# Kernel optimization log

Measured on AMD Instinct MI355X. Metric: run time of the kernel, lower is better.

## Reference

```python
import jax, jax.numpy as jnp
import numpy as np

N_AXIS = 128      # n_x_axis == n_y_axis
N_TARGET = 8192


def setup_inputs() -> dict:
    key = jax.random.key(0)
    k1, k2 = jax.random.split(key, 2)
    # decoder output feature map: (4, n_y, n_x)
    feature_map = jax.random.normal(k1, (4, N_AXIS, N_AXIS), dtype=jnp.float32)
    # encoder grid: regular 2d grid in [-3, 3]^2, flattened (n_x*n_y, 2)
    ax = jnp.linspace(-3.0, 3.0, N_AXIS, dtype=jnp.float32)
    gx, gy = jnp.meshgrid(ax, ax, indexing='ij')
    grid = jnp.stack([gx, gy], axis=-1).reshape(N_AXIS * N_AXIS, 2)
    # target points in the same domain
    X_target = jax.random.uniform(k2, (N_TARGET, 2), dtype=jnp.float32,
                                  minval=-3.0, maxval=3.0)
    l_scale = jnp.float32(1.0)
    return {"feature_map": feature_map, "grid": grid,
            "X_target": X_target, "l_scale": l_scale}


def reference(feature_map, grid, X_target, l_scale):
    n_y, n_x = feature_map.shape[1], feature_map.shape[2]
    # Means_grid = FM[:2].permute(2,1,0).reshape(n_x*n_y, 2)
    means_grid = jnp.transpose(feature_map[:2], (2, 1, 0)).reshape(n_x * n_y, 2)
    # Sigmas_grid = softplus(FM[2:]), same permute/reshape
    sigmas_grid = jnp.transpose(jax.nn.softplus(feature_map[2:]), (2, 1, 0)).reshape(n_x * n_y, 2)
    # RBF kernel between targets and grid: K[t,g] = exp(-||xt-xg||^2 / (2 l^2))
    d2 = jnp.sum((X_target[:, None, :] - grid[None, :, :]) ** 2, axis=-1)  # [T, G]
    K = jnp.exp(-0.5 * d2 / (l_scale ** 2))
    denom = jnp.sum(K, axis=1, keepdims=True)  # normalized (Nadaraya-Watson)
    means_target = (K @ means_grid) / denom    # [T, 2]
    sigmas_target = (K @ sigmas_grid) / denom  # [T, 2]
    return means_target, sigmas_target
```

## Files before the change

### kernel.cpp

```cpp
#include <hip/hip_runtime.h>
#include <hip/hip_bf16.h>
#include <math.h>


#define NA      128
#define TT      16
#define THREADS 512

typedef __attribute__((ext_vector_type(8))) short short8;
typedef __attribute__((ext_vector_type(4))) float f32x4;

__device__ __forceinline__ short f2bf(float x) {
    __hip_bfloat16 h = __float2bfloat16(x);
    return *reinterpret_cast<short*>(&h);
}

__global__ __launch_bounds__(256)
void pack_pre(const float* __restrict__ fm, short* __restrict__ bfB)
{
    const int idx = blockIdx.x * 256 + threadIdx.x;
    if (idx >= 8192) return;
    const int L = idx & 63;
    const int s = (idx >> 6) & 3;
    const int n = (idx >> 8) & 7;
    const int c = idx >> 11;
    const int i  = n * 16 + (L & 15);
    const int k0 = s * 32 + (L >> 4) * 8;
    const float* src = fm + c * NA * NA;

    short8 o;
#pragma unroll
    for (int e = 0; e < 8; ++e) {
        float x = src[(k0 + e) * NA + i];
        if (c >= 2) x = (x > 15.0f) ? x : log1pf(__expf(x));
        o[e] = f2bf(x);
    }
    *reinterpret_cast<short8*>(&bfB[idx * 8]) = o;
}

__global__ __launch_bounds__(THREADS)
void cnp_mfma(const short* __restrict__ bfB,
              const float* __restrict__ grid,
              const float* __restrict__ xt,
              const float* __restrict__ lsp,
              float* __restrict__ out,
              int n_target)
{
    __shared__ __attribute__((aligned(16))) float Kx[TT * NA];
    __shared__ __attribute__((aligned(16))) short kyA[4 * 64 * 8];
    __shared__ float psx[TT][2], psy[TT][2];
    __shared__ float red[4][2][TT];

    const int tid  = threadIdx.x;
    const int wid  = tid >> 6;
    const int c    = wid & 3;
    const int nh   = wid >> 2;
    const int lane = tid & 63;
    const int t0   = blockIdx.x * TT;

    const float l      = lsp[0];
    const float inv2l2 = 0.5f / (l * l);

#pragma unroll
    for (int s = 0; s < 4; ++s) {
        const int k = s * THREADS + tid;
        const int t = k >> 7;
        const int j = k & 127;
        int tg = t0 + t; if (tg >= n_target) tg = n_target - 1;
        const float ax = grid[j * 2 + 1];
        const float dx = xt[tg * 2 + 0] - ax;
        const float dy = xt[tg * 2 + 1] - ax;
        const float kxv = __expf(-dx * dx * inv2l2);
        const float kyv = __expf(-dy * dy * inv2l2);
        Kx[t * NA + j] = kxv;
        const int ss = j >> 5, g = (j & 31) >> 3, e = j & 7;
        kyA[((ss * 64) + g * 16 + (t & 15)) * 8 + e] = f2bf(kyv);
        float sx = kxv, sy = kyv;
        sx += __shfl_xor(sx, 1);  sy += __shfl_xor(sy, 1);
        sx += __shfl_xor(sx, 2);  sy += __shfl_xor(sy, 2);
        sx += __shfl_xor(sx, 4);  sy += __shfl_xor(sy, 4);
        sx += __shfl_xor(sx, 8);  sy += __shfl_xor(sy, 8);
        sx += __shfl_xor(sx, 16); sy += __shfl_xor(sy, 16);
        sx += __shfl_xor(sx, 32); sy += __shfl_xor(sy, 32);
        if (lane == 0) {
            const int half = (k >> 6) & 1;
            psx[t][half] = sx;
            psy[t][half] = sy;
        }
    }
    __syncthreads();

    const short8* kap = reinterpret_cast<const short8*>(kyA);
    const short8 a0 = kap[0 * 64 + lane];
    const short8 a1 = kap[1 * 64 + lane];
    const short8 a2 = kap[2 * 64 + lane];
    const short8 a3 = kap[3 * 64 + lane];

    const short8* bbase = reinterpret_cast<const short8*>(bfB)
                        + c * 2048 + nh * 4 * 256 + lane;
    const int icol = lane & 15;
    const int tb   = (lane >> 4) * 4;
    f32x4 p = {0.f, 0.f, 0.f, 0.f};

#pragma unroll
    for (int nn = 0; nn < 4; ++nn) {
        const short8* bp = bbase + nn * 256;
        f32x4 acc = {0.f, 0.f, 0.f, 0.f};
        acc = __builtin_amdgcn_mfma_f32_16x16x32_bf16(a0, bp[0],   acc, 0, 0, 0);
        acc = __builtin_amdgcn_mfma_f32_16x16x32_bf16(a1, bp[64],  acc, 0, 0, 0);
        acc = __builtin_amdgcn_mfma_f32_16x16x32_bf16(a2, bp[128], acc, 0, 0, 0);
        acc = __builtin_amdgcn_mfma_f32_16x16x32_bf16(a3, bp[192], acc, 0, 0, 0);
        const int i = (nh * 4 + nn) * 16 + icol;
        p.x = fmaf(Kx[(tb + 0) * NA + i], acc.x, p.x);
        p.y = fmaf(Kx[(tb + 1) * NA + i], acc.y, p.y);
        p.z = fmaf(Kx[(tb + 2) * NA + i], acc.z, p.z);
        p.w = fmaf(Kx[(tb + 3) * NA + i], acc.w, p.w);
    }

#pragma unroll
    for (int st = 1; st <= 8; st <<= 1) {
        p.x += __shfl_xor(p.x, st);
        p.y += __shfl_xor(p.y, st);
        p.z += __shfl_xor(p.z, st);
        p.w += __shfl_xor(p.w, st);
    }
    if ((lane & 15) == 0) {
        red[c][nh][tb + 0] = p.x;
        red[c][nh][tb + 1] = p.y;
        red[c][nh][tb + 2] = p.z;
        red[c][nh][tb + 3] = p.w;
    }
    __syncthreads();

    if (tid < 4 * TT) {
        const int t  = tid & (TT - 1);
        const int cc = tid >> 4;
        const int tg = t0 + t;
        if (tg < n_target) {
            const float numer = red[cc][0][t] + red[cc][1][t];
            const float Sx = psx[t][0] + psx[t][1];
            const float Sy = psy[t][0] + psy[t][1];
            const float val = numer / (Sx * Sy);
            if (cc < 2) out[tg * 2 + cc] = val;
            else        out[n_target * 2 + tg * 2 + (cc - 2)] = val;
        }
    }
}

extern "C" void kernel_launch(void* const* d_in, const int* in_sizes, int n_in,
                              void* d_out, int out_size, void* d_ws, size_t ws_size,
                              hipStream_t stream) {
    const float* fm   = (const float*)d_in[0];
    const float* grid = (const float*)d_in[1];
    const float* xt   = (const float*)d_in[2];
    const float* lsp  = (const float*)d_in[3];
    float* out = (float*)d_out;
    short* bfB = (short*)d_ws;

    const int n_target = in_sizes[2] / 2;

    hipLaunchKernelGGL(pack_pre, dim3(32), dim3(256), 0, stream, fm, bfB);

    const int blocks = (n_target + TT - 1) / TT;
    hipLaunchKernelGGL(cnp_mfma, dim3(blocks), dim3(THREADS), 0, stream,
                       bfB, grid, xt, lsp, out, n_target);
}
```

Measured before the change: 18.05 us.

## Coalesce pack_pre reads and move denominator sums to an LDS reduction pass

pack_pre now has each thread read a coalesced float4 from the feature map and scatter four bf16 values into the MFMA B layout, with twice as many threads. It replaces the old strided 8-element column reads and vector store. In the main kernel, the per-iteration 64-lane shuffle reductions for the row sums are removed. Ky is also kept in fp32 shared memory, and after the barrier a separate pass reduces each row with 16-lane groups. This trades an extra 8 KB of LDS and scattered 2-byte global writes for fewer shuffles and better read coalescing.

After: 16.14 us. -10.6%, faster.

```diff
diff --git a/kernel.cpp b/kernel.cpp
--- a/kernel.cpp
+++ b/kernel.cpp
@@ -19,23 +19,28 @@
 void pack_pre(const float* __restrict__ fm, short* __restrict__ bfB)
 {
     const int idx = blockIdx.x * 256 + threadIdx.x;
-    if (idx >= 8192) return;
-    const int L = idx & 63;
-    const int s = (idx >> 6) & 3;
-    const int n = (idx >> 8) & 7;
-    const int c = idx >> 11;
-    const int i  = n * 16 + (L & 15);
-    const int k0 = s * 32 + (L >> 4) * 8;
-    const float* src = fm + c * NA * NA;
+    const int c  = idx >> 12;
+    const int k  = (idx >> 5) & 127;
+    const int i0 = (idx & 31) * 4;
 
-    short8 o;
+    float4 v = *reinterpret_cast<const float4*>(fm + c * NA * NA + k * NA + i0);
+    if (c >= 2) {
+        v.x = (v.x > 15.0f) ? v.x : log1pf(__expf(v.x));
+        v.y = (v.y > 15.0f) ? v.y : log1pf(__expf(v.y));
+        v.z = (v.z > 15.0f) ? v.z : log1pf(__expf(v.z));
+        v.w = (v.w > 15.0f) ? v.w : log1pf(__expf(v.w));
+    }
+    const int s = k >> 5;
+    const int e = k & 7;
+    const int Lk = ((k >> 3) & 3) * 16;
+    const float vv[4] = {v.x, v.y, v.z, v.w};
 #pragma unroll
-    for (int e = 0; e < 8; ++e) {
-        float x = src[(k0 + e) * NA + i];
-        if (c >= 2) x = (x > 15.0f) ? x : log1pf(__expf(x));
-        o[e] = f2bf(x);
+    for (int d = 0; d < 4; ++d) {
+        const int i = i0 + d;
+        const int n = i >> 4;
+        const int L = Lk + (i & 15);
+        bfB[(((c * 8 + n) * 4 + s) * 64 + L) * 8 + e] = f2bf(vv[d]);
     }
-    *reinterpret_cast<short8*>(&bfB[idx * 8]) = o;
 }
 
 __global__ __launch_bounds__(THREADS)
@@ -47,8 +52,9 @@
               int n_target)
 {
     __shared__ __attribute__((aligned(16))) float Kx[TT * NA];
+    __shared__ __attribute__((aligned(16))) float Ky32[TT * NA];
     __shared__ __attribute__((aligned(16))) short kyA[4 * 64 * 8];
-    __shared__ float psx[TT][2], psy[TT][2];
+    __shared__ float psx[TT], psy[TT];
     __shared__ float red[4][2][TT];
 
     const int tid  = threadIdx.x;
@@ -72,23 +78,26 @@
         const float dy = xt[tg * 2 + 1] - ax;
         const float kxv = __expf(-dx * dx * inv2l2);
         const float kyv = __expf(-dy * dy * inv2l2);
-        Kx[t * NA + j] = kxv;
+        Kx[t * NA + j]   = kxv;
+        Ky32[t * NA + j] = kyv;
         const int ss = j >> 5, g = (j & 31) >> 3, e = j & 7;
         kyA[((ss * 64) + g * 16 + (t & 15)) * 8 + e] = f2bf(kyv);
-        float sx = kxv, sy = kyv;
-        sx += __shfl_xor(sx, 1);  sy += __shfl_xor(sy, 1);
-        sx += __shfl_xor(sx, 2);  sy += __shfl_xor(sy, 2);
-        sx += __shfl_xor(sx, 4);  sy += __shfl_xor(sy, 4);
-        sx += __shfl_xor(sx, 8);  sy += __shfl_xor(sy, 8);
-        sx += __shfl_xor(sx, 16); sy += __shfl_xor(sy, 16);
-        sx += __shfl_xor(sx, 32); sy += __shfl_xor(sy, 32);
-        if (lane == 0) {
-            const int half = (k >> 6) & 1;
-            psx[t][half] = sx;
-            psy[t][half] = sy;
-        }
     }
     __syncthreads();
+
+    {
+        const int grp  = tid >> 4;
+        const int l16  = tid & 15;
+        const int t    = grp >> 1;
+        const int axis = grp & 1;
+        const float* kb = axis ? Ky32 : Kx;
+        const float4 q0 = *reinterpret_cast<const float4*>(&kb[t * NA + l16 * 8]);
+        const float4 q1 = *reinterpret_cast<const float4*>(&kb[t * NA + l16 * 8 + 4]);
+        float u = ((q0.x + q0.y) + (q0.z + q0.w)) + ((q1.x + q1.y) + (q1.z + q1.w));
+        u += __shfl_xor(u, 1); u += __shfl_xor(u, 2);
+        u += __shfl_xor(u, 4); u += __shfl_xor(u, 8);
+        if (l16 == 0) { if (axis) psy[t] = u; else psx[t] = u; }
+    }
 
     const short8* kap = reinterpret_cast<const short8*>(kyA);
     const short8 a0 = kap[0 * 64 + lane];
@@ -138,9 +147,7 @@
         const int tg = t0 + t;
         if (tg < n_target) {
             const float numer = red[cc][0][t] + red[cc][1][t];
-            const float Sx = psx[t][0] + psx[t][1];
-            const float Sy = psy[t][0] + psy[t][1];
-            const float val = numer / (Sx * Sy);
+            const float val = numer / (psx[t] * psy[t]);
             if (cc < 2) out[tg * 2 + cc] = val;
             else        out[n_target * 2 + tg * 2 + (cc - 2)] = val;
         }
@@ -159,7 +166,7 @@
 
     const int n_target = in_sizes[2] / 2;
 
-    hipLaunchKernelGGL(pack_pre, dim3(32), dim3(256), 0, stream, fm, bfB);
+    hipLaunchKernelGGL(pack_pre, dim3(64), dim3(256), 0, stream, fm, bfB);
 
     const int blocks = (n_target + TT - 1) / TT;
     hipLaunchKernelGGL(cnp_mfma, dim3(blocks), dim3(THREADS), 0, stream,
```
